# Kernel tuning notes

Hardware: AMD Instinct MI355X
Metric: run time of the kernel (lower is better)

Reference implementation:

```python
import jax, jax.numpy as jnp
import numpy as np

D_MODEL = 2048
D_FF = 8192
EPS = 1e-5


def layernorm(x, g, b):
    m = x.mean(-1, keepdims=True)
    v = ((x - m) ** 2).mean(-1, keepdims=True)
    return (x - m) * jax.lax.rsqrt(v + EPS) * g + b


def rotate_half(x):
    return jnp.concatenate([-x[..., ::2], x[..., 1::2]], axis=-1)


def sinu_pos_emb(dim, length):
    inv_freq = 1.0 / 10000 ** (jnp.arange(0, dim, 2, dtype=jnp.float32) / dim)
    pos = jnp.arange(length, dtype=jnp.float32)
    sp = pos[:, None] * inv_freq[None, :]           # [S, dim/2]
    return jnp.concatenate([jnp.sin(sp), jnp.cos(sp)], axis=-1)  # [S, dim]


def setup_inputs() -> dict:
    key = jax.random.key(0)
    ks = jax.random.split(key, 10)
    d, f = D_MODEL, D_FF
    sc = 0.02
    return {
        "src":  jax.random.normal(ks[0], (4, 2048, d), jnp.float32),
        "Wqkv": jax.random.normal(ks[1], (3 * d, d), jnp.float32) * sc,
        "bqkv": jnp.zeros((3 * d,), jnp.float32),
        "Wo":   jax.random.normal(ks[2], (d, d), jnp.float32) * sc,
        "bo":   jnp.zeros((d,), jnp.float32),
        "W1":   jax.random.normal(ks[3], (f, d), jnp.float32) * sc,
        "b1":   jnp.zeros((f,), jnp.float32),
        "W2":   jax.random.normal(ks[4], (d, f), jnp.float32) * sc,
        "b2":   jnp.zeros((d,), jnp.float32),
        "g1":   jnp.ones((d,), jnp.float32),
        "be1":  jnp.zeros((d,), jnp.float32),
        "g2":   jnp.ones((d,), jnp.float32),
        "be2":  jnp.zeros((d,), jnp.float32),
    }


def reference(src, Wqkv, bqkv, Wo, bo, W1, b1, W2, b2, g1, be1, g2, be2):
    B, S, d = src.shape
    # norm1 (note: torch code reassigns src, so residuals use the normed value)
    src = layernorm(src, g1, be1)
    qkv = src @ Wqkv.T + bqkv                      # [B,S,3d]
    Q, K, V = qkv[..., :d], qkv[..., d:2 * d], qkv[..., 2 * d:]
    # rotary: cos/sin of the (sin,cos)-concatenated table, faithful to source
    emb = sinu_pos_emb(d, S)                       # [S,d]
    c, s = jnp.cos(emb), jnp.sin(emb)
    Q = Q * c + rotate_half(Q) * s
    K = K * c - rotate_half(K) * s
    # causal SDPA over full d_model (no head split in source)
    scale = 1.0 / jnp.sqrt(jnp.float32(d))
    scores = jnp.einsum('bqd,bkd->bqk', Q, K) * scale
    causal = jnp.tril(jnp.ones((S, S), bool))
    scores = jnp.where(causal, scores, jnp.float32(-1e30))
    P = jax.nn.softmax(scores, axis=-1)
    attn = jnp.einsum('bqk,bkd->bqd', P, V)
    src = src + attn @ Wo.T + bo
    # FFN block
    h = layernorm(src, g2, be2)
    h = jax.nn.relu(h @ W1.T + b1) @ W2.T + b2
    return src + h
```

## Files before the change

### kernel.cpp

```cpp
#include <hip/hip_runtime.h>
#include <cstdint>


typedef __attribute__((ext_vector_type(8))) short short8;
typedef __attribute__((ext_vector_type(4))) float floatx4;

#define PLANE 16777216L
#define SS    4194304L

__device__ __forceinline__ float bf2f(unsigned short u) {
    union { unsigned int i; float f; } v; v.i = ((unsigned int)u) << 16; return v.f;
}
__device__ __forceinline__ unsigned short f2bf(float f) {
    union { float f; unsigned int i; } v; v.f = f;
    unsigned int x = v.i;
    return (unsigned short)((x + 0x7FFFu + ((x >> 16) & 1u)) >> 16);
}
__device__ __forceinline__ uint4 pack8(float4 a, float4 b) {
    unsigned short o[8];
    o[0] = f2bf(a.x); o[1] = f2bf(a.y); o[2] = f2bf(a.z); o[3] = f2bf(a.w);
    o[4] = f2bf(b.x); o[5] = f2bf(b.y); o[6] = f2bf(b.z); o[7] = f2bf(b.w);
    return *(uint4*)o;
}
__device__ __forceinline__ void gl_lds16(const void* g, void* l) {
    __builtin_amdgcn_global_load_lds(
        (const __attribute__((address_space(1))) void*)g,
        (__attribute__((address_space(3))) void*)l, 16, 0, 0);
}

#define EM_QKV  0
#define EM_SC   1
#define EM_PV   2
#define EM_PROJ 3
#define EM_FFN1 4
#define EM_F2A  5

template<int EM>
__launch_bounds__(256, 2)
__global__ void gemm_bt(const unsigned short* __restrict__ A,
                        const unsigned short* __restrict__ B,
                        void* __restrict__ Cv, int N, int K,
                        const float* __restrict__ bias,
                        const unsigned short* __restrict__ resid16,
                        unsigned short* __restrict__ outQ,
                        unsigned short* __restrict__ outVt)
{
    constexpr int BM = 128, BN = 128, BK = 32;
    __shared__ __align__(16) unsigned short As[BM * BK];
    __shared__ __align__(16) unsigned short Bs[BN * BK];

    const int m0 = blockIdx.x * BM, n0 = blockIdx.y * BN;
    if (EM == EM_SC && n0 > m0 + (BM - 1)) return;

    int kmax = K;
    if (EM == EM_PV) { kmax = m0 + BM; if (kmax > K) kmax = K; }
    const int nsteps = kmax / BK;

    const int t = threadIdx.x;
    const int lane = t & 63, wave = t >> 6;
    const int q = lane >> 4, ln = lane & 15;
    const int wm = (wave >> 1) * 64, wn = (wave & 1) * 64;

    const int r0 = wave * 32;
    const int rA = r0 + (lane >> 2);
    const int cslot = lane & 3;
    const int cg0 = (cslot ^ (rA & 3)) * 8;
    const int cg1 = (cslot ^ ((rA + 16) & 3)) * 8;
    const unsigned short* Agp0 = A + (long)(m0 + rA) * K + cg0;
    const unsigned short* Agp1 = A + (long)(m0 + rA + 16) * K + cg1;
    const unsigned short* Bgp0 = B + (long)(n0 + rA) * K + cg0;
    const unsigned short* Bgp1 = B + (long)(n0 + rA + 16) * K + cg1;
    unsigned short* lA0 = &As[r0 * 32];
    unsigned short* lA1 = &As[(r0 + 16) * 32];
    unsigned short* lB0 = &Bs[r0 * 32];
    unsigned short* lB1 = &Bs[(r0 + 16) * 32];

    floatx4 acc[4][4];
#pragma unroll
    for (int i = 0; i < 4; ++i)
#pragma unroll
        for (int j = 0; j < 4; ++j) acc[i][j] = (floatx4){0.f, 0.f, 0.f, 0.f};

    for (int s = 0; s < nsteps; ++s) {
        const long off = (long)s * BK;
        __syncthreads();
        gl_lds16(Agp0 + off, lA0);
        gl_lds16(Agp1 + off, lA1);
        gl_lds16(Bgp0 + off, lB0);
        gl_lds16(Bgp1 + off, lB1);
        __syncthreads();
        short8 af[4], bfr[4];
#pragma unroll
        for (int i = 0; i < 4; ++i) {
            const int R = wm + 16 * i + ln;
            af[i] = *(const short8*)&As[R * 32 + ((q ^ (R & 3)) * 8)];
        }
#pragma unroll
        for (int j = 0; j < 4; ++j) {
            const int R = wn + 16 * j + ln;
            bfr[j] = *(const short8*)&Bs[R * 32 + ((q ^ (R & 3)) * 8)];
        }
#pragma unroll
        for (int i = 0; i < 4; ++i)
#pragma unroll
            for (int j = 0; j < 4; ++j)
                acc[i][j] = __builtin_amdgcn_mfma_f32_16x16x32_bf16(af[i], bfr[j], acc[i][j], 0, 0, 0);
    }

#pragma unroll
    for (int i = 0; i < 4; ++i) {
#pragma unroll
        for (int r = 0; r < 4; ++r) {
            const int row = m0 + wm + 16 * i + q * 4 + r;
#pragma unroll
            for (int j = 0; j < 4; ++j) {
                const int col = n0 + wn + 16 * j + ln;
                float v = acc[i][j][r];
                const long idx = (long)row * N + col;
                if constexpr (EM == EM_SC) {
                    ((unsigned short*)Cv)[idx] = f2bf(v);
                } else if constexpr (EM == EM_PV) {
                    ((unsigned short*)Cv)[idx] = f2bf(v);
                }
            }
        }
    }
}

#define BARM()   do { __builtin_amdgcn_s_barrier(); asm volatile("" ::: "memory"); } while (0)
#define LGKM(n)  asm volatile("s_waitcnt lgkmcnt(" #n ")" ::: "memory")
#define VMCNT(n) asm volatile("s_waitcnt vmcnt(" #n ")" ::: "memory")
#define PRIO1()  __builtin_amdgcn_s_setprio(1)
#define PRIO0()  __builtin_amdgcn_s_setprio(0)

template<int EM>
__launch_bounds__(512, 2)
__global__ void gemm256(const unsigned short* __restrict__ A,
                        const unsigned short* __restrict__ B,
                        void* __restrict__ Cv, int N, int K,
                        const float* __restrict__ bias,
                        const unsigned short* __restrict__ resid16,
                        unsigned short* __restrict__ outQ,
                        unsigned short* __restrict__ outVt)
{
    __shared__ __align__(16) unsigned short As[2][16384];
    __shared__ __align__(16) unsigned short Bs[2][16384];

    const int m0 = blockIdx.x * 256, n0 = blockIdx.y * 256;
    const int t = threadIdx.x;
    const int lane = t & 63, wave = t >> 6;
    const int q = lane >> 4, ln = lane & 15;
    const int wm = wave >> 2, wn = wave & 3;

    const int jrow = lane >> 3;
    const int csrc = ((lane & 7) ^ jrow) * 8;
    const unsigned short* Ag = A + (long)(m0 + wave * 16 + jrow) * K + csrc;
    const unsigned short* Bg = B + (long)(n0 + wave * 16 + jrow) * K + csrc;
    const int ldsSlice = wave * 1024;

    const int aBase = (wm * 128 + ln) * 64;
    const int bBase = (wn * 64 + ln) * 64;
    const int c0 = ((0 + q) ^ (ln & 7)) * 8;
    const int c1 = ((4 + q) ^ (ln & 7)) * 8;

    floatx4 acc[8][4];
#pragma unroll
    for (int i = 0; i < 8; ++i)
#pragma unroll
        for (int j = 0; j < 4; ++j) acc[i][j] = (floatx4){0.f, 0.f, 0.f, 0.f};

    short8 a0r[4][2], a1r[4][2];
    short8 b0r[2][2], b1r[2][2];

#define STAGE_A(buf, kt, h) do { \
    const unsigned short* _g = Ag + (long)((h) * 128) * K + ((long)(kt) << 6); \
    gl_lds16(_g,          &As[buf][(h) * 8192 + ldsSlice]); \
    gl_lds16(_g + 8L * K, &As[buf][(h) * 8192 + ldsSlice + 512]); \
} while (0)
#define STAGE_B(buf, kt, h) do { \
    const unsigned short* _g = Bg + (long)((h) * 128) * K + ((long)(kt) << 6); \
    gl_lds16(_g,          &Bs[buf][(h) * 8192 + ldsSlice]); \
    gl_lds16(_g + 8L * K, &Bs[buf][(h) * 8192 + ldsSlice + 512]); \
} while (0)
#define RD_A0F(sel, i) { \
    a0r[i][0] = *(const short8*)&As[sel][aBase + (16 * (i)) * 64 + c0]; \
    a0r[i][1] = *(const short8*)&As[sel][aBase + (16 * (i)) * 64 + c1]; }
#define RD_A1F(sel, i) { \
    a1r[i][0] = *(const short8*)&As[sel][aBase + (64 + 16 * (i)) * 64 + c0]; \
    a1r[i][1] = *(const short8*)&As[sel][aBase + (64 + 16 * (i)) * 64 + c1]; }
#define RD_B0A(sel) { \
    _Pragma("unroll") \
    for (int j = 0; j < 2; ++j) { \
        b0r[j][0] = *(const short8*)&Bs[sel][bBase + (16 * j) * 64 + c0]; \
        b0r[j][1] = *(const short8*)&Bs[sel][bBase + (16 * j) * 64 + c1]; } }
#define RD_B1A(sel) { \
    _Pragma("unroll") \
    for (int j = 0; j < 2; ++j) { \
        b1r[j][0] = *(const short8*)&Bs[sel][bBase + (32 + 16 * j) * 64 + c0]; \
        b1r[j][1] = *(const short8*)&Bs[sel][bBase + (32 + 16 * j) * 64 + c1]; } }
#define MMQ(ar, br, mg, ng) { \
    _Pragma("unroll") \
    for (int i = 0; i < 4; ++i) \
    _Pragma("unroll") \
    for (int j = 0; j < 2; ++j) { \
        acc[(mg)*4+i][(ng)*2+j] = __builtin_amdgcn_mfma_f32_16x16x32_bf16( \
            ar[i][0], br[j][0], acc[(mg)*4+i][(ng)*2+j], 0, 0, 0); \
        acc[(mg)*4+i][(ng)*2+j] = __builtin_amdgcn_mfma_f32_16x16x32_bf16( \
            ar[i][1], br[j][1], acc[(mg)*4+i][(ng)*2+j], 0, 0, 0); \
    } }

    const int NG = K >> 6;

    STAGE_A(0, 0, 0); STAGE_A(0, 0, 1);
    STAGE_B(0, 0, 0); STAGE_B(0, 0, 1);
    STAGE_B(1, 1, 0);
    STAGE_A(1, 1, 0);
    VMCNT(4); BARM();
    RD_A0F(0, 0); RD_A0F(0, 1); RD_A0F(0, 2); RD_A0F(0, 3);
    RD_B0A(0);

    for (int g = 0; g < NG - 2; ++g) {
        const int cur = g & 1, nxt = cur ^ 1;
        RD_B1A(cur); RD_A1F(cur, 0);
        STAGE_A(nxt, g + 1, 1);
        LGKM(6);
        PRIO1(); MMQ(a0r, b0r, 0, 0); PRIO0();
        BARM();
        RD_A1F(cur, 1); RD_A1F(cur, 2); RD_A1F(cur, 3);
        STAGE_B(nxt, g + 1, 1);
        LGKM(6);
        PRIO1(); MMQ(a0r, b1r, 0, 1); PRIO0();
        VMCNT(2); BARM();
        RD_A0F(nxt, 0); RD_A0F(nxt, 1); RD_A0F(nxt, 2);
        STAGE_B(cur, g + 2, 0);
        LGKM(6);
        PRIO1(); MMQ(a1r, b0r, 1, 0); PRIO0();
        VMCNT(2); BARM();
        RD_A0F(nxt, 3); RD_B0A(nxt);
        STAGE_A(cur, g + 2, 0);
        LGKM(6);
        PRIO1(); MMQ(a1r, b1r, 1, 1); PRIO0();
        BARM();
    }
    {
        const int g = NG - 2, cur = g & 1, nxt = cur ^ 1;
        RD_B1A(cur); RD_A1F(cur, 0);
        STAGE_A(nxt, g + 1, 1);
        LGKM(6);
        PRIO1(); MMQ(a0r, b0r, 0, 0); PRIO0();
        BARM();
        RD_A1F(cur, 1); RD_A1F(cur, 2); RD_A1F(cur, 3);
        STAGE_B(nxt, g + 1, 1);
        LGKM(6);
        PRIO1(); MMQ(a0r, b1r, 0, 1); PRIO0();
        VMCNT(2); BARM();
        RD_A0F(nxt, 0); RD_A0F(nxt, 1); RD_A0F(nxt, 2);
        LGKM(6);
        PRIO1(); MMQ(a1r, b0r, 1, 0); PRIO0();
        VMCNT(0); BARM();
        RD_A0F(nxt, 3); RD_B0A(nxt);
        LGKM(6);
        PRIO1(); MMQ(a1r, b1r, 1, 1); PRIO0();
        BARM();
    }
    {
        const int cur = (NG - 1) & 1;
        RD_B1A(cur); RD_A1F(cur, 0);
        LGKM(6);
        PRIO1(); MMQ(a0r, b0r, 0, 0); PRIO0();
        RD_A1F(cur, 1); RD_A1F(cur, 2); RD_A1F(cur, 3);
        LGKM(6);
        PRIO1(); MMQ(a0r, b1r, 0, 1); PRIO0();
        LGKM(0);
        PRIO1(); MMQ(a1r, b0r, 1, 0); PRIO0();
        PRIO1(); MMQ(a1r, b1r, 1, 1); PRIO0();
    }

#undef STAGE_A
#undef STAGE_B
#undef RD_A0F
#undef RD_A1F
#undef RD_B0A
#undef RD_B1A
#undef MMQ

#pragma unroll
    for (int i = 0; i < 8; ++i) {
#pragma unroll
        for (int r = 0; r < 4; ++r) {
            const int row = m0 + wm * 128 + 16 * i + q * 4 + r;
#pragma unroll
            for (int j = 0; j < 4; ++j) {
                const int col = n0 + wn * 64 + 16 * j + ln;
                float v = acc[i][j][r];
                const long idx = (long)row * N + col;
                if constexpr (EM == EM_QKV) {
                    v += bias[col];
                    const unsigned short vb = f2bf(v);
                    const int p = col >> 11, c2 = col & 2047;
                    if (p == 0)      outQ[(long)row * 2048 + c2] = vb;
                    else if (p == 1) (outQ + PLANE)[(long)row * 2048 + c2] = vb;
                    else             outVt[(long)(row >> 11) * SS + (long)c2 * 2048 + (row & 2047)] = vb;
                } else if constexpr (EM == EM_PROJ) {
                    v += bias[col] + bf2f(resid16[idx]);
                    ((float*)Cv)[idx] = v;
                } else if constexpr (EM == EM_FFN1) {
                    v = fmaxf(v + bias[col], 0.f);
                    ((unsigned short*)Cv)[idx] = f2bf(v);
                } else {
                    ((float*)Cv)[idx] += v;
                }
            }
        }
    }
}

__launch_bounds__(256)
__global__ void cvt_rows(const float* __restrict__ src, unsigned short* __restrict__ dst, long srcld)
{
    const int row = blockIdx.x, t = threadIdx.x;
    const float* s = src + (long)row * srcld + t * 8;
    float4 a = *(const float4*)s;
    float4 b = *(const float4*)(s + 4);
    *(uint4*)(dst + (long)row * 2048 + t * 8) = pack8(a, b);
}

__launch_bounds__(256)
__global__ void layernorm_k(const float* __restrict__ X, unsigned short* __restrict__ Y,
                            const float* __restrict__ g, const float* __restrict__ be)
{
    const int row = blockIdx.x, t = threadIdx.x;
    const float* Xr = X + (long)row * 2048 + t * 8;
    float4 v0 = *(const float4*)Xr;
    float4 v1 = *(const float4*)(Xr + 4);
    float x[8] = {v0.x, v0.y, v0.z, v0.w, v1.x, v1.y, v1.z, v1.w};
    float s = 0.f, ss = 0.f;
#pragma unroll
    for (int k = 0; k < 8; ++k) { s += x[k]; ss += x[k] * x[k]; }
    for (int off = 32; off; off >>= 1) { s += __shfl_down(s, off, 64); ss += __shfl_down(ss, off, 64); }
    __shared__ float red[8];
    const int wave = t >> 6, lane = t & 63;
    if (lane == 0) { red[wave] = s; red[4 + wave] = ss; }
    __syncthreads();
    s  = red[0] + red[1] + red[2] + red[3];
    ss = red[4] + red[5] + red[6] + red[7];
    const float mean = s * (1.f / 2048.f);
    const float var  = ss * (1.f / 2048.f) - mean * mean;
    const float rstd = rsqrtf(var + 1e-5f);
    unsigned short o[8];
#pragma unroll
    for (int k = 0; k < 8; ++k) {
        const int col = t * 8 + k;
        o[k] = f2bf((x[k] - mean) * rstd * g[col] + be[col]);
    }
    *(uint4*)(Y + (long)row * 2048 + t * 8) = *(uint4*)o;
}

__launch_bounds__(256)
__global__ void rope_inplace(unsigned short* __restrict__ Q, unsigned short* __restrict__ K)
{
    __shared__ __align__(16) unsigned short rowbuf[2048];
    const int row = blockIdx.x;
    const int mtx = blockIdx.y;
    unsigned short* X = (mtx ? K : Q) + (long)row * 2048;
    const int t = threadIdx.x;
    *(uint4*)&rowbuf[t * 8] = *(const uint4*)(X + t * 8);
    __syncthreads();
    const int p = row & 2047;
    const float sgn = mtx ? -1.f : 1.f;
    unsigned short o[8];
#pragma unroll
    for (int e = 0; e < 8; ++e) {
        const int j = t * 8 + e;
        const int i = j & 1023;
        const float freq = __expf(-(float)i * (9.210340371976184f / 1024.0f));
        const float sp = (float)p * freq;
        const float emb = (j < 1024) ? sinf(sp) : cosf(sp);
        float se, ce;
        sincosf(emb, &se, &ce);
        const int pj = (j < 1024) ? (2 * j) : (2 * j - 2047);
        float xp = bf2f(rowbuf[pj]);
        if (j < 1024) xp = -xp;
        o[e] = f2bf(bf2f(rowbuf[j]) * ce + sgn * xp * se);
    }
    *(uint4*)(X + t * 8) = *(uint4*)o;
}

__launch_bounds__(256)
__global__ void softmax_causal(unsigned short* __restrict__ S)
{
    const int qq = blockIdx.x;
    const int L = qq + 1;
    unsigned short* srow = S + (long)qq * 2048;
    const int t = threadIdx.x;
    const float scale = 0.022097086912079608f;
    float vals[8];
    float m = -1e30f;
#pragma unroll
    for (int u = 0; u < 8; ++u) {
        const int i2 = t + 256 * u;
        vals[u] = (i2 < L) ? bf2f(srow[i2]) * scale : -1e30f;
        m = fmaxf(m, vals[u]);
    }
    for (int off = 32; off; off >>= 1) m = fmaxf(m, __shfl_down(m, off, 64));
    __shared__ float red[8];
    const int wave = t >> 6, lane = t & 63;
    if (lane == 0) red[wave] = m;
    __syncthreads();
    m = fmaxf(fmaxf(red[0], red[1]), fmaxf(red[2], red[3]));
    float sum = 0.f;
#pragma unroll
    for (int u = 0; u < 8; ++u) {
        float e = __expf(vals[u] - m);
        e = (t + 256 * u < L) ? e : 0.f;
        vals[u] = e; sum += e;
    }
    for (int off = 32; off; off >>= 1) sum += __shfl_down(sum, off, 64);
    if (lane == 0) red[4 + wave] = sum;
    __syncthreads();
    sum = red[4] + red[5] + red[6] + red[7];
    const float inv = 1.0f / sum;
#pragma unroll
    for (int u = 0; u < 8; ++u) srow[t + 256 * u] = f2bf(vals[u] * inv);
}

__launch_bounds__(256)
__global__ void final_add(float* __restrict__ io, const float* __restrict__ b2)
{
    const int row = blockIdx.x, t = threadIdx.x;
    const long base = (long)row * 2048 + t * 8;
    float4 a0 = *(const float4*)(io + base);
    float4 a1 = *(const float4*)(io + base + 4);
    float4 c0 = *(const float4*)(b2 + t * 8);
    float4 c1 = *(const float4*)(b2 + t * 8 + 4);
    a0.x += c0.x; a0.y += c0.y; a0.z += c0.z; a0.w += c0.w;
    a1.x += c1.x; a1.y += c1.y; a1.z += c1.z; a1.w += c1.w;
    *(float4*)(io + base) = a0;
    *(float4*)(io + base + 4) = a1;
}

extern "C" void kernel_launch(void* const* d_in, const int* in_sizes, int n_in,
                              void* d_out, int out_size, void* d_ws, size_t ws_size,
                              hipStream_t stream)
{
    const float* src  = (const float*)d_in[0];
    const float* Wqkv = (const float*)d_in[1];
    const float* bqkv = (const float*)d_in[2];
    const float* Wo   = (const float*)d_in[3];
    const float* bo   = (const float*)d_in[4];
    const float* W1   = (const float*)d_in[5];
    const float* b1   = (const float*)d_in[6];
    const float* W2   = (const float*)d_in[7];
    const float* b2   = (const float*)d_in[8];
    const float* g1   = (const float*)d_in[9];
    const float* be1  = (const float*)d_in[10];
    const float* g2   = (const float*)d_in[11];
    const float* be2  = (const float*)d_in[12];

    char* ws = (char*)d_ws;
    const long MB = 1LL << 20;
    unsigned short* x1    = (unsigned short*)ws;
    unsigned short* Vt    = (unsigned short*)(ws + 32 * MB);
    unsigned short* Wqbf  = (unsigned short*)(ws + 64 * MB);
    unsigned short* attn  = (unsigned short*)(ws + 64 * MB);
    unsigned short* scP   = (unsigned short*)(ws + 96 * MB);
    unsigned short* Wobf  = (unsigned short*)(ws + 96 * MB);
    unsigned short* W1c   = (unsigned short*)(ws + 96 * MB);
    unsigned short* W2c   = (unsigned short*)(ws + 104 * MB);
    unsigned short* h2    = x1;
    unsigned short* f1    = Vt;

    unsigned short* Q    = (unsigned short*)d_out;
    float*          src2 = (float*)d_out;
    float*          out  = (float*)d_out;

    const dim3 blk(256);
    const dim3 blk512(512);

    cvt_rows<<<6144, blk, 0, stream>>>(Wqkv, Wqbf, 2048);
    layernorm_k<<<8192, blk, 0, stream>>>(src, x1, g1, be1);
    gemm256<EM_QKV><<<dim3(32, 24), blk512, 0, stream>>>(
        x1, Wqbf, nullptr, 6144, 2048, bqkv, nullptr, Q, Vt);
    rope_inplace<<<dim3(8192, 2), blk, 0, stream>>>(Q, Q + PLANE);

    for (int b = 0; b < 4; ++b) {
        gemm_bt<EM_SC><<<dim3(16, 16), blk, 0, stream>>>(
            Q + b * SS, Q + PLANE + b * SS, scP, 2048, 2048, nullptr, nullptr, nullptr, nullptr);
        softmax_causal<<<2048, blk, 0, stream>>>(scP);
        gemm_bt<EM_PV><<<dim3(16, 16), blk, 0, stream>>>(
            scP, Vt + b * SS, attn + b * SS, 2048, 2048, nullptr, nullptr, nullptr, nullptr);
    }

    cvt_rows<<<2048, blk, 0, stream>>>(Wo, Wobf, 2048);
    gemm256<EM_PROJ><<<dim3(32, 8), blk512, 0, stream>>>(
        attn, Wobf, src2, 2048, 2048, bo, x1, nullptr, nullptr);
    layernorm_k<<<8192, blk, 0, stream>>>(src2, h2, g2, be2);

    for (int c = 0; c < 4; ++c) {
        cvt_rows<<<2048, blk, 0, stream>>>(W1 + (long)c * 2048 * 2048, W1c, 2048);
        cvt_rows<<<2048, blk, 0, stream>>>(W2 + (long)c * 2048, W2c, 8192);
        gemm256<EM_FFN1><<<dim3(32, 8), blk512, 0, stream>>>(
            h2, W1c, f1, 2048, 2048, b1 + c * 2048, nullptr, nullptr, nullptr);
        gemm256<EM_F2A><<<dim3(32, 8), blk512, 0, stream>>>(
            f1, W2c, src2, 2048, 2048, nullptr, nullptr, nullptr, nullptr);
    }
    final_add<<<8192, blk, 0, stream>>>(out, b2);
}
```

Baseline: 1.660 ms.

## Restructure GEMM mainloop to HipKittens-style 8-wave ping-pong with single A register set

Rewrites the 256x256 bf16 GEMM mainloop so each quarter-step issues one global->LDS stage plus its LDS fragment reads, then crosses a barrier, waits on lgkmcnt(0) and runs an MFMA cluster guarded by a sched_barrier. It also changes the staging address mapping so a block's threads cover contiguous 64-row slabs, and uses one A register set instead of two. This aims to cut register pressure and give a cleaner alternation between memory and MFMA phases across waves. In exchange it adds more barriers and full lgkm waits, which can serialize the LDS reads against the MFMAs.

New measurement: 1.674 ms. Within noise of the previous version (+0.8%).

```diff
diff --git a/kernel.cpp b/kernel.cpp
--- a/kernel.cpp
+++ b/kernel.cpp
@@ -128,8 +128,9 @@
 }
 
 #define BARM()   do { __builtin_amdgcn_s_barrier(); asm volatile("" ::: "memory"); } while (0)
-#define LGKM(n)  asm volatile("s_waitcnt lgkmcnt(" #n ")" ::: "memory")
+#define LGKM0()  asm volatile("s_waitcnt lgkmcnt(0)" ::: "memory")
 #define VMCNT(n) asm volatile("s_waitcnt vmcnt(" #n ")" ::: "memory")
+#define SCHEDB() __builtin_amdgcn_sched_barrier(0)
 #define PRIO1()  __builtin_amdgcn_s_setprio(1)
 #define PRIO0()  __builtin_amdgcn_s_setprio(0)
 
@@ -152,11 +153,11 @@
     const int q = lane >> 4, ln = lane & 15;
     const int wm = wave >> 2, wn = wave & 3;
 
-    const int jrow = lane >> 3;
-    const int csrc = ((lane & 7) ^ jrow) * 8;
-    const unsigned short* Ag = A + (long)(m0 + wave * 16 + jrow) * K + csrc;
-    const unsigned short* Bg = B + (long)(n0 + wave * 16 + jrow) * K + csrc;
-    const int ldsSlice = wave * 1024;
+    const int srow = t >> 3;
+    const int csrcS = ((t & 7) ^ (srow & 7)) * 8;
+    const unsigned short* AgS = A + (long)(m0 + srow) * K + csrcS;
+    const unsigned short* BgS = B + (long)(n0 + srow) * K + csrcS;
+    const int wslice = wave * 512;
 
     const int aBase = (wm * 128 + ln) * 64;
     const int bBase = (wn * 64 + ln) * 64;
@@ -169,119 +170,115 @@
 #pragma unroll
         for (int j = 0; j < 4; ++j) acc[i][j] = (floatx4){0.f, 0.f, 0.f, 0.f};
 
-    short8 a0r[4][2], a1r[4][2];
+    short8 a[4][2];
     short8 b0r[2][2], b1r[2][2];
 
 #define STAGE_A(buf, kt, h) do { \
-    const unsigned short* _g = Ag + (long)((h) * 128) * K + ((long)(kt) << 6); \
-    gl_lds16(_g,          &As[buf][(h) * 8192 + ldsSlice]); \
-    gl_lds16(_g + 8L * K, &As[buf][(h) * 8192 + ldsSlice + 512]); \
+    const unsigned short* _g = AgS + (long)((h) * 128) * K + ((long)(kt) << 6); \
+    gl_lds16(_g,           &As[buf][(h) * 8192 + wslice]); \
+    gl_lds16(_g + 64L * K, &As[buf][(h) * 8192 + 4096 + wslice]); \
 } while (0)
 #define STAGE_B(buf, kt, h) do { \
-    const unsigned short* _g = Bg + (long)((h) * 128) * K + ((long)(kt) << 6); \
-    gl_lds16(_g,          &Bs[buf][(h) * 8192 + ldsSlice]); \
-    gl_lds16(_g + 8L * K, &Bs[buf][(h) * 8192 + ldsSlice + 512]); \
+    const unsigned short* _g = BgS + (long)((h) * 128) * K + ((long)(kt) << 6); \
+    gl_lds16(_g,           &Bs[buf][(h) * 8192 + wslice]); \
+    gl_lds16(_g + 64L * K, &Bs[buf][(h) * 8192 + 4096 + wslice]); \
 } while (0)
-#define RD_A0F(sel, i) { \
-    a0r[i][0] = *(const short8*)&As[sel][aBase + (16 * (i)) * 64 + c0]; \
-    a0r[i][1] = *(const short8*)&As[sel][aBase + (16 * (i)) * 64 + c1]; }
-#define RD_A1F(sel, i) { \
-    a1r[i][0] = *(const short8*)&As[sel][aBase + (64 + 16 * (i)) * 64 + c0]; \
-    a1r[i][1] = *(const short8*)&As[sel][aBase + (64 + 16 * (i)) * 64 + c1]; }
-#define RD_B0A(sel) { \
+#define RD_A(sel, mg) { \
+    _Pragma("unroll") \
+    for (int i = 0; i < 4; ++i) { \
+        a[i][0] = *(const short8*)&As[sel][aBase + ((mg) * 64 + 16 * i) * 64 + c0]; \
+        a[i][1] = *(const short8*)&As[sel][aBase + ((mg) * 64 + 16 * i) * 64 + c1]; \
+    } }
+#define RD_B0(sel) { \
     _Pragma("unroll") \
     for (int j = 0; j < 2; ++j) { \
         b0r[j][0] = *(const short8*)&Bs[sel][bBase + (16 * j) * 64 + c0]; \
         b0r[j][1] = *(const short8*)&Bs[sel][bBase + (16 * j) * 64 + c1]; } }
-#define RD_B1A(sel) { \
+#define RD_B1(sel) { \
     _Pragma("unroll") \
     for (int j = 0; j < 2; ++j) { \
         b1r[j][0] = *(const short8*)&Bs[sel][bBase + (32 + 16 * j) * 64 + c0]; \
         b1r[j][1] = *(const short8*)&Bs[sel][bBase + (32 + 16 * j) * 64 + c1]; } }
-#define MMQ(ar, br, mg, ng) { \
+#define MMQ(mg, br, ng) { \
     _Pragma("unroll") \
     for (int i = 0; i < 4; ++i) \
     _Pragma("unroll") \
     for (int j = 0; j < 2; ++j) { \
         acc[(mg)*4+i][(ng)*2+j] = __builtin_amdgcn_mfma_f32_16x16x32_bf16( \
-            ar[i][0], br[j][0], acc[(mg)*4+i][(ng)*2+j], 0, 0, 0); \
+            a[i][0], br[j][0], acc[(mg)*4+i][(ng)*2+j], 0, 0, 0); \
         acc[(mg)*4+i][(ng)*2+j] = __builtin_amdgcn_mfma_f32_16x16x32_bf16( \
-            ar[i][1], br[j][1], acc[(mg)*4+i][(ng)*2+j], 0, 0, 0); \
+            a[i][1], br[j][1], acc[(mg)*4+i][(ng)*2+j], 0, 0, 0); \
     } }
 
     const int NG = K >> 6;
 
     STAGE_A(0, 0, 0); STAGE_A(0, 0, 1);
     STAGE_B(0, 0, 0); STAGE_B(0, 0, 1);
-    STAGE_B(1, 1, 0);
     STAGE_A(1, 1, 0);
-    VMCNT(4); BARM();
-    RD_A0F(0, 0); RD_A0F(0, 1); RD_A0F(0, 2); RD_A0F(0, 3);
-    RD_B0A(0);
+    VMCNT(2); BARM();
 
     for (int g = 0; g < NG - 2; ++g) {
         const int cur = g & 1, nxt = cur ^ 1;
-        RD_B1A(cur); RD_A1F(cur, 0);
         STAGE_A(nxt, g + 1, 1);
-        LGKM(6);
-        PRIO1(); MMQ(a0r, b0r, 0, 0); PRIO0();
+        RD_A(cur, 0); RD_B0(cur);
+        BARM(); LGKM0(); SCHEDB();
+        PRIO1(); MMQ(0, b0r, 0); PRIO0();
         BARM();
-        RD_A1F(cur, 1); RD_A1F(cur, 2); RD_A1F(cur, 3);
+        STAGE_B(nxt, g + 1, 0);
+        RD_B1(cur);
+        BARM(); LGKM0(); SCHEDB();
+        PRIO1(); MMQ(0, b1r, 1); PRIO0();
+        BARM();
         STAGE_B(nxt, g + 1, 1);
-        LGKM(6);
-        PRIO1(); MMQ(a0r, b1r, 0, 1); PRIO0();
+        RD_A(cur, 1);
+        BARM(); LGKM0(); SCHEDB();
+        PRIO1(); MMQ(1, b0r, 0); PRIO0();
+        BARM();
+        STAGE_A(cur, g + 2, 0);
+        BARM(); SCHEDB();
+        PRIO1(); MMQ(1, b1r, 1); PRIO0();
         VMCNT(2); BARM();
-        RD_A0F(nxt, 0); RD_A0F(nxt, 1); RD_A0F(nxt, 2);
-        STAGE_B(cur, g + 2, 0);
-        LGKM(6);
-        PRIO1(); MMQ(a1r, b0r, 1, 0); PRIO0();
-        VMCNT(2); BARM();
-        RD_A0F(nxt, 3); RD_B0A(nxt);
-        STAGE_A(cur, g + 2, 0);
-        LGKM(6);
-        PRIO1(); MMQ(a1r, b1r, 1, 1); PRIO0();
-        BARM();
     }
     {
         const int g = NG - 2, cur = g & 1, nxt = cur ^ 1;
-        RD_B1A(cur); RD_A1F(cur, 0);
         STAGE_A(nxt, g + 1, 1);
-        LGKM(6);
-        PRIO1(); MMQ(a0r, b0r, 0, 0); PRIO0();
+        RD_A(cur, 0); RD_B0(cur);
+        BARM(); LGKM0(); SCHEDB();
+        PRIO1(); MMQ(0, b0r, 0); PRIO0();
         BARM();
-        RD_A1F(cur, 1); RD_A1F(cur, 2); RD_A1F(cur, 3);
+        STAGE_B(nxt, g + 1, 0);
+        RD_B1(cur);
+        BARM(); LGKM0(); SCHEDB();
+        PRIO1(); MMQ(0, b1r, 1); PRIO0();
+        BARM();
         STAGE_B(nxt, g + 1, 1);
-        LGKM(6);
-        PRIO1(); MMQ(a0r, b1r, 0, 1); PRIO0();
-        VMCNT(2); BARM();
-        RD_A0F(nxt, 0); RD_A0F(nxt, 1); RD_A0F(nxt, 2);
-        LGKM(6);
-        PRIO1(); MMQ(a1r, b0r, 1, 0); PRIO0();
+        RD_A(cur, 1);
+        BARM(); LGKM0(); SCHEDB();
+        PRIO1(); MMQ(1, b0r, 0); PRIO0();
+        BARM();
+        SCHEDB();
+        PRIO1(); MMQ(1, b1r, 1); PRIO0();
         VMCNT(0); BARM();
-        RD_A0F(nxt, 3); RD_B0A(nxt);
-        LGKM(6);
-        PRIO1(); MMQ(a1r, b1r, 1, 1); PRIO0();
-        BARM();
     }
     {
         const int cur = (NG - 1) & 1;
-        RD_B1A(cur); RD_A1F(cur, 0);
-        LGKM(6);
-        PRIO1(); MMQ(a0r, b0r, 0, 0); PRIO0();
-        RD_A1F(cur, 1); RD_A1F(cur, 2); RD_A1F(cur, 3);
-        LGKM(6);
-        PRIO1(); MMQ(a0r, b1r, 0, 1); PRIO0();
-        LGKM(0);
-        PRIO1(); MMQ(a1r, b0r, 1, 0); PRIO0();
-        PRIO1(); MMQ(a1r, b1r, 1, 1); PRIO0();
+        RD_A(cur, 0); RD_B0(cur);
+        LGKM0(); SCHEDB();
+        PRIO1(); MMQ(0, b0r, 0); PRIO0();
+        RD_B1(cur);
+        LGKM0(); SCHEDB();
+        PRIO1(); MMQ(0, b1r, 1); PRIO0();
+        RD_A(cur, 1);
+        LGKM0(); SCHEDB();
+        PRIO1(); MMQ(1, b0r, 0); PRIO0();
+        PRIO1(); MMQ(1, b1r, 1); PRIO0();
     }
 
 #undef STAGE_A
 #undef STAGE_B
-#undef RD_A0F
-#undef RD_A1F
-#undef RD_B0A
-#undef RD_B1A
+#undef RD_A
+#undef RD_B0
+#undef RD_B1
 #undef MMQ
 
 #pragma unroll
```
